# Performance work log

Measured on AMD Instinct MI355X. Metric: run time of the kernel, lower is better.

## Reference

```python
import jax, jax.numpy as jnp
import numpy as np


def setup_inputs() -> dict:
    key = jax.random.key(0)
    ks = jax.random.split(key, 6)
    B, S, F = 8, 2048, 1024
    scale = 1.0 / np.sqrt(F)
    return {
        "query": jax.random.normal(ks[0], (B, S, F), dtype=jnp.float32),
        "key": jax.random.normal(ks[1], (B, S, F), dtype=jnp.float32),
        "value": jax.random.normal(ks[2], (B, S, F), dtype=jnp.float32),
        "Wq": jax.random.normal(ks[3], (F, F), dtype=jnp.float32) * scale,
        "Wk": jax.random.normal(ks[4], (F, F), dtype=jnp.float32) * scale,
        "Wv": jax.random.normal(ks[5], (F, F), dtype=jnp.float32) * scale,
    }


def reference(query, key, value, Wq, Wk, Wv):
    # nn.Linear(bias=False): x @ W.T, W is [out, in]
    q_t = jnp.einsum('bsf,gf->bsg', query, Wq)
    k_t = jnp.einsum('bsf,gf->bsg', key, Wk)
    v_t = jnp.einsum('bsf,gf->bsg', value, Wv)
    F = k_t.shape[-1]
    scale = jnp.asarray(1.0, q_t.dtype) / jnp.sqrt(jnp.asarray(F, q_t.dtype))
    attn = jnp.einsum('bij,bkj->bik', q_t, k_t) * scale  # [B, S, S]
    # original uses nn.Softmax(dim=1): softmax over the query (i) axis
    attn = jax.nn.softmax(attn, axis=1)
    # 'bii,bij->bij': diagonal of attn scales rows of v_t
    diag = jnp.diagonal(attn, axis1=1, axis2=2)  # [B, S]
    proj = diag[:, :, None] * v_t  # [B, S, F]
    return proj
```

## Files before the change

### kernel.cpp

```cpp
#include <hip/hip_runtime.h>


typedef _Float16 f16x8 __attribute__((ext_vector_type(8)));
typedef float    f32x4 __attribute__((ext_vector_type(4)));

#define COLIC 8
#define SCALE 0.03125f

typedef __attribute__((address_space(1))) const unsigned int g_u32_t;
typedef __attribute__((address_space(3))) unsigned int l_u32_t;

__device__ __forceinline__ void gload16(const _Float16* g, _Float16* l) {
  __builtin_amdgcn_global_load_lds((g_u32_t*)g, (l_u32_t*)l, 16, 0, 0);
}

__device__ __forceinline__ void stage_tile64(const _Float16* gbase, int ldk,
                                             _Float16* lds, int w, int lane) {
#pragma unroll
  for (int c = 0; c < 4; ++c) {
    const int blk = c * 4 + w;
    const int o = (blk << 10) + (lane << 4);
    const int row = o >> 7;
    const int colb = (o & 127) ^ ((row & 7) << 4);
    gload16(gbase + (size_t)row * ldk + (colb >> 1), lds + (blk << 9));
  }
}

struct Conv3Args {
  const float* src[3];
  _Float16* dst[3];
};
__global__ __launch_bounds__(256)
void conv3_f32_f16(Conv3Args a, int n8) {
  const float* __restrict__ src = a.src[blockIdx.y];
  _Float16* __restrict__ dst = a.dst[blockIdx.y];
  for (int i = blockIdx.x * 256 + threadIdx.x; i < n8; i += gridDim.x * 256) {
    const float4 x = ((const float4*)src)[2 * i];
    const float4 y = ((const float4*)src)[2 * i + 1];
    f16x8 o;
    o[0] = (_Float16)x.x; o[1] = (_Float16)x.y;
    o[2] = (_Float16)x.z; o[3] = (_Float16)x.w;
    o[4] = (_Float16)y.x; o[5] = (_Float16)y.y;
    o[6] = (_Float16)y.z; o[7] = (_Float16)y.w;
    ((f16x8*)dst)[i] = o;
  }
}

struct Conv2Args {
  const float* src[2];
  _Float16* dst[2];
};
__global__ __launch_bounds__(256)
void convT_f32_f16(Conv2Args a) {
  __shared__ float Ts[64][65];
  const float* __restrict__ src = a.src[blockIdx.z];
  _Float16* __restrict__ dst = a.dst[blockIdx.z];
  const int g0 = blockIdx.x * 64, f0 = blockIdx.y * 64;
  const int tid = threadIdx.x;
  {
    const int r = tid >> 4;
    const int c4 = (tid & 15) << 2;
#pragma unroll
    for (int p = 0; p < 4; ++p) {
      const int row = p * 16 + r;
      const float4 v = *(const float4*)&src[(size_t)(g0 + row) * 1024 + f0 + c4];
      Ts[row][c4 + 0] = v.x; Ts[row][c4 + 1] = v.y;
      Ts[row][c4 + 2] = v.z; Ts[row][c4 + 3] = v.w;
    }
  }
  __syncthreads();
  {
    const int f = tid >> 3;
    const int gs = (tid & 7) << 3;
#pragma unroll
    for (int p = 0; p < 2; ++p) {
      const int fr = p * 32 + f;
      f16x8 v;
#pragma unroll
      for (int j = 0; j < 8; ++j) v[j] = (_Float16)Ts[gs + j][fr];
      *(f16x8*)&dst[(size_t)(f0 + fr) * 1024 + g0 + gs] = v;
    }
  }
}

template <int F16OUT>
__global__ __launch_bounds__(256)
void gemm_mfma(const _Float16* __restrict__ A, const _Float16* __restrict__ B,
               _Float16* __restrict__ C16, float* __restrict__ C32,
               const float* __restrict__ mpart, const float* __restrict__ lpart,
               const float* __restrict__ sdiag, int BSz,
               int M, int N, int Kd) {
  __shared__ __align__(16) _Float16 As[128 * 64];
  __shared__ __align__(16) _Float16 Bs[128 * 64];
  __shared__ float diagS[128];
  const int tid = threadIdx.x;
  const int w = tid >> 6, lane = tid & 63;
  const int wr = w >> 1, wc = w & 1;
  const int lr = lane & 15, kq = lane >> 4;
  const int swz = (lr & 7) << 4;
  const int bm = blockIdx.x * 128, bn = blockIdx.y * 128;

  if (!F16OUT && tid < 128) {
    const int row = bm + tid;
    float Mx = -3.0e38f;
#pragma unroll
    for (int c = 0; c < COLIC; ++c) Mx = fmaxf(Mx, mpart[(size_t)c * BSz + row]);
    float L = 0.0f;
#pragma unroll
    for (int c = 0; c < COLIC; ++c)
      L += lpart[(size_t)c * BSz + row] * __expf(mpart[(size_t)c * BSz + row] - Mx);
    diagS[tid] = __expf(sdiag[row] - Mx) / L;
  }

  f32x4 acc[4][4] = {};
  for (int k0 = 0; k0 < Kd; k0 += 64) {
    stage_tile64(A + (size_t)bm * Kd + k0, Kd, As, w, lane);
    stage_tile64(B + (size_t)bn * Kd + k0, Kd, Bs, w, lane);
    __syncthreads();
    f16x8 af[4][2], bf[4][2];
#pragma unroll
    for (int mi = 0; mi < 4; ++mi) {
      const int ro = (wr * 64 + mi * 16 + lr) << 7;
      af[mi][0] = *(const f16x8*)&As[(ro + ((kq * 16) ^ swz)) >> 1];
      af[mi][1] = *(const f16x8*)&As[(ro + ((64 + kq * 16) ^ swz)) >> 1];
    }
#pragma unroll
    for (int ni = 0; ni < 4; ++ni) {
      const int ro = (wc * 64 + ni * 16 + lr) << 7;
      bf[ni][0] = *(const f16x8*)&Bs[(ro + ((kq * 16) ^ swz)) >> 1];
      bf[ni][1] = *(const f16x8*)&Bs[(ro + ((64 + kq * 16) ^ swz)) >> 1];
    }
#pragma unroll
    for (int ks = 0; ks < 2; ++ks)
#pragma unroll
      for (int mi = 0; mi < 4; ++mi)
#pragma unroll
        for (int ni = 0; ni < 4; ++ni)
          acc[mi][ni] = __builtin_amdgcn_mfma_f32_16x16x32_f16(af[mi][ks], bf[ni][ks], acc[mi][ni], 0, 0, 0);
    __syncthreads();
  }
#pragma unroll
  for (int mi = 0; mi < 4; ++mi) {
#pragma unroll
    for (int j = 0; j < 4; ++j) {
      const int rloc = wr * 64 + mi * 16 + kq * 4 + j;
      const int row = bm + rloc;
      float s = 1.0f;
      if (!F16OUT) s = diagS[rloc];
#pragma unroll
      for (int ni = 0; ni < 4; ++ni) {
        const int col = bn + wc * 64 + ni * 16 + lr;
        if (F16OUT) C16[(size_t)row * N + col] = (_Float16)acc[mi][ni][j];
        else        C32[(size_t)row * N + col] = acc[mi][ni][j] * s;
      }
    }
  }
}

__global__ __launch_bounds__(256)
void col_stats_mfma(const _Float16* __restrict__ qt, const _Float16* __restrict__ kt,
                    float* __restrict__ mpart, float* __restrict__ lpart,
                    float* __restrict__ sdiag, int S, int Fd, int chunk) {
  __shared__ __align__(16) _Float16 Qs[128 * 64];
  __shared__ __align__(16) _Float16 Ks[128 * 64];
  __shared__ float redM[8][128];
  __shared__ float redL[8][128];
  const int t = blockIdx.x + 16 * (blockIdx.y + 8 * blockIdx.z);
  const int jb = ((t & 7) << 1) | ((t >> 3) & 1);
  const int rr = t >> 4;
  const int ic = rr & 7;
  const int b  = rr >> 3;
  const int j0 = jb * 128;
  const _Float16* Q = qt + (size_t)b * S * Fd;
  const _Float16* K = kt + (size_t)b * S * Fd;
  const int tid = threadIdx.x;
  const int w = tid >> 6, lane = tid & 63;
  const int wr = w >> 1, wc = w & 1;
  const int lr = lane & 15, kq = lane >> 4;
  const int swz = (lr & 7) << 4;

  float m[4], l[4];
#pragma unroll
  for (int ni = 0; ni < 4; ++ni) { m[ni] = -3.0e38f; l[ni] = 0.0f; }

  for (int it = 0; it < chunk >> 7; ++it) {
    const int i0 = ic * chunk + (it << 7);
    f32x4 acc[4][4] = {};
    for (int k0 = 0; k0 < Fd; k0 += 64) {
      stage_tile64(Q + (size_t)i0 * Fd + k0, Fd, Qs, w, lane);
      stage_tile64(K + (size_t)j0 * Fd + k0, Fd, Ks, w, lane);
      __syncthreads();
      f16x8 af[4][2], bf[4][2];
#pragma unroll
      for (int mi = 0; mi < 4; ++mi) {
        const int ro = (wr * 64 + mi * 16 + lr) << 7;
        af[mi][0] = *(const f16x8*)&Qs[(ro + ((kq * 16) ^ swz)) >> 1];
        af[mi][1] = *(const f16x8*)&Qs[(ro + ((64 + kq * 16) ^ swz)) >> 1];
      }
#pragma unroll
      for (int ni = 0; ni < 4; ++ni) {
        const int ro = (wc * 64 + ni * 16 + lr) << 7;
        bf[ni][0] = *(const f16x8*)&Ks[(ro + ((kq * 16) ^ swz)) >> 1];
        bf[ni][1] = *(const f16x8*)&Ks[(ro + ((64 + kq * 16) ^ swz)) >> 1];
      }
#pragma unroll
      for (int ks = 0; ks < 2; ++ks)
#pragma unroll
        for (int mi = 0; mi < 4; ++mi)
#pragma unroll
          for (int ni = 0; ni < 4; ++ni)
            acc[mi][ni] = __builtin_amdgcn_mfma_f32_16x16x32_f16(af[mi][ks], bf[ni][ks], acc[mi][ni], 0, 0, 0);
      __syncthreads();
    }
    if (i0 == j0 && wr == wc && (lr >> 2) == kq) {
      const int j = lr & 3;
#pragma unroll
      for (int jj = 0; jj < 4; ++jj)
        sdiag[(size_t)b * S + j0 + wc * 64 + jj * 16 + lr] = acc[jj][jj][j] * SCALE;
    }
#pragma unroll
    for (int ni = 0; ni < 4; ++ni) {
      float tm = -3.0e38f;
#pragma unroll
      for (int mi = 0; mi < 4; ++mi)
#pragma unroll
        for (int jj = 0; jj < 4; ++jj) tm = fmaxf(tm, acc[mi][ni][jj]);
      tm *= SCALE;
      const float mn = fmaxf(m[ni], tm);
      float add = 0.0f;
#pragma unroll
      for (int mi = 0; mi < 4; ++mi)
#pragma unroll
        for (int jj = 0; jj < 4; ++jj) add += __expf(acc[mi][ni][jj] * SCALE - mn);
      l[ni] = l[ni] * __expf(m[ni] - mn) + add;
      m[ni] = mn;
    }
  }
  __syncthreads();
  const int p = wr * 4 + kq;
#pragma unroll
  for (int ni = 0; ni < 4; ++ni) {
    const int col = wc * 64 + ni * 16 + lr;
    redM[p][col] = m[ni];
    redL[p][col] = l[ni];
  }
  __syncthreads();
  if (tid < 128) {
    float M = -3.0e38f;
#pragma unroll
    for (int q = 0; q < 8; ++q) M = fmaxf(M, redM[q][tid]);
    float L = 0.0f;
#pragma unroll
    for (int q = 0; q < 8; ++q) L += redL[q][tid] * __expf(redM[q][tid] - M);
    const size_t idx = ((size_t)ic * 8 + b) * S + j0 + tid;
    mpart[idx] = M;
    lpart[idx] = L;
  }
}

extern "C" void kernel_launch(void* const* d_in, const int* in_sizes, int n_in,
                              void* d_out, int out_size, void* d_ws, size_t ws_size,
                              hipStream_t stream) {
  const float* query = (const float*)d_in[0];
  const float* key   = (const float*)d_in[1];
  const float* value = (const float*)d_in[2];
  const float* Wq    = (const float*)d_in[3];
  const float* Wk    = (const float*)d_in[4];
  const float* Wv    = (const float*)d_in[5];

  const int F = 1024;
  const int BS = in_sizes[0] / F;
  const int B = 8;
  const int S = BS / B;

  _Float16* q16   = (_Float16*)d_ws;
  _Float16* k16   = q16 + (size_t)BS * F;
  _Float16* v16   = k16 + (size_t)BS * F;
  _Float16* wqT16 = v16 + (size_t)BS * F;
  _Float16* wkT16 = wqT16 + (size_t)F * F;
  _Float16* wv16  = wkT16 + (size_t)F * F;
  _Float16* W2h   = wv16 + (size_t)F * F;
  float* mpart = (float*)(W2h + (size_t)F * F);
  float* lpart = mpart + (size_t)COLIC * BS;
  float* sdiag = lpart + (size_t)COLIC * BS;

  _Float16* kt2 = (_Float16*)d_out;

  const dim3 blk(256);
  const int n8x = BS * F / 8, n8w = F * F / 8;

  Conv3Args ax; ax.src[0] = query; ax.src[1] = key; ax.src[2] = value;
  ax.dst[0] = q16; ax.dst[1] = k16; ax.dst[2] = v16;
  conv3_f32_f16<<<dim3(2048, 3), blk, 0, stream>>>(ax, n8x);

  Conv3Args av; av.src[0] = Wv; av.dst[0] = wv16;
  conv3_f32_f16<<<dim3(512, 1), blk, 0, stream>>>(av, n8w);

  Conv2Args at; at.src[0] = Wq; at.src[1] = Wk;
  at.dst[0] = wqT16; at.dst[1] = wkT16;
  convT_f32_f16<<<dim3(16, 16, 2), blk, 0, stream>>>(at);

  gemm_mfma<1><<<dim3(8, 8), blk, 0, stream>>>(wqT16, wkT16, W2h, (float*)nullptr,
                                               (const float*)nullptr, (const float*)nullptr,
                                               (const float*)nullptr, 0, F, F, F);

  gemm_mfma<1><<<dim3(BS / 128, F / 128), blk, 0, stream>>>(k16, W2h, kt2, (float*)nullptr,
                                               (const float*)nullptr, (const float*)nullptr,
                                               (const float*)nullptr, 0, BS, F, F);

  const dim3 sgrid(S / 128, COLIC, B);
  col_stats_mfma<<<sgrid, blk, 0, stream>>>(q16, kt2, mpart, lpart, sdiag,
                                            S, F, S / COLIC);

  gemm_mfma<0><<<dim3(BS / 128, F / 128), blk, 0, stream>>>(v16, wv16, (_Float16*)nullptr,
                                               (float*)d_out, mpart, lpart, sdiag,
                                               BS, BS, F, F);
}
```

Before: 270.8 us.

## Widen col_stats tiles to 256 key columns with 512-thread blocks

The column-statistics kernel now covers 256 key columns per block using 8 waves (2x4) instead of 128 columns with 4 waves, so each staged Q tile is reused across twice as many key columns. Staging, the diagonal extraction and the per-column reduction are adapted to the wider tile, and the custom block-index swizzle is dropped in favour of a plain grid mapping. This halves redundant Q loads but raises LDS use and block size, which can lower occupancy and changes L2 locality.

New measurement: 275.7 us. Within noise of the previous version (+1.8%).

```diff
diff --git a/kernel.cpp b/kernel.cpp
--- a/kernel.cpp
+++ b/kernel.cpp
@@ -19,6 +19,19 @@
 #pragma unroll
   for (int c = 0; c < 4; ++c) {
     const int blk = c * 4 + w;
+    const int o = (blk << 10) + (lane << 4);
+    const int row = o >> 7;
+    const int colb = (o & 127) ^ ((row & 7) << 4);
+    gload16(gbase + (size_t)row * ldk + (colb >> 1), lds + (blk << 9));
+  }
+}
+
+template <int CH>
+__device__ __forceinline__ void stage_rows8(const _Float16* gbase, int ldk,
+                                            _Float16* lds, int w8, int lane) {
+#pragma unroll
+  for (int c = 0; c < CH; ++c) {
+    const int blk = c * 8 + w8;
     const int o = (blk << 10) + (lane << 4);
     const int row = o >> 7;
     const int colb = (o & 127) ^ ((row & 7) << 4);
@@ -157,25 +170,21 @@
   }
 }
 
-__global__ __launch_bounds__(256)
+__global__ __launch_bounds__(512)
 void col_stats_mfma(const _Float16* __restrict__ qt, const _Float16* __restrict__ kt,
                     float* __restrict__ mpart, float* __restrict__ lpart,
                     float* __restrict__ sdiag, int S, int Fd, int chunk) {
   __shared__ __align__(16) _Float16 Qs[128 * 64];
-  __shared__ __align__(16) _Float16 Ks[128 * 64];
-  __shared__ float redM[8][128];
-  __shared__ float redL[8][128];
-  const int t = blockIdx.x + 16 * (blockIdx.y + 8 * blockIdx.z);
-  const int jb = ((t & 7) << 1) | ((t >> 3) & 1);
-  const int rr = t >> 4;
-  const int ic = rr & 7;
-  const int b  = rr >> 3;
-  const int j0 = jb * 128;
+  __shared__ __align__(16) _Float16 Ks[256 * 64];
+  __shared__ float redM[8][256];
+  __shared__ float redL[8][256];
+  const int b = blockIdx.z, jb = blockIdx.x, ic = blockIdx.y;
+  const int j0b = jb * 256;
   const _Float16* Q = qt + (size_t)b * S * Fd;
   const _Float16* K = kt + (size_t)b * S * Fd;
   const int tid = threadIdx.x;
   const int w = tid >> 6, lane = tid & 63;
-  const int wr = w >> 1, wc = w & 1;
+  const int wr = w >> 2, wc = w & 3;
   const int lr = lane & 15, kq = lane >> 4;
   const int swz = (lr & 7) << 4;
 
@@ -187,8 +196,8 @@
     const int i0 = ic * chunk + (it << 7);
     f32x4 acc[4][4] = {};
     for (int k0 = 0; k0 < Fd; k0 += 64) {
-      stage_tile64(Q + (size_t)i0 * Fd + k0, Fd, Qs, w, lane);
-      stage_tile64(K + (size_t)j0 * Fd + k0, Fd, Ks, w, lane);
+      stage_rows8<2>(Q + (size_t)i0 * Fd + k0, Fd, Qs, w, lane);
+      stage_rows8<4>(K + (size_t)j0b * Fd + k0, Fd, Ks, w, lane);
       __syncthreads();
       f16x8 af[4][2], bf[4][2];
 #pragma unroll
@@ -212,11 +221,14 @@
             acc[mi][ni] = __builtin_amdgcn_mfma_f32_16x16x32_f16(af[mi][ks], bf[ni][ks], acc[mi][ni], 0, 0, 0);
       __syncthreads();
     }
-    if (i0 == j0 && wr == wc && (lr >> 2) == kq) {
-      const int j = lr & 3;
-#pragma unroll
-      for (int jj = 0; jj < 4; ++jj)
-        sdiag[(size_t)b * S + j0 + wc * 64 + jj * 16 + lr] = acc[jj][jj][j] * SCALE;
+    if (i0 >= j0b && i0 < j0b + 256) {
+      const int jh = (i0 - j0b) >> 7;
+      if ((wc >> 1) == jh && (wc & 1) == wr && (lr >> 2) == kq) {
+        const int j = lr & 3;
+#pragma unroll
+        for (int mi = 0; mi < 4; ++mi)
+          sdiag[(size_t)b * S + j0b + wc * 64 + mi * 16 + lr] = acc[mi][mi][j] * SCALE;
+      }
     }
 #pragma unroll
     for (int ni = 0; ni < 4; ++ni) {
@@ -245,14 +257,14 @@
     redL[p][col] = l[ni];
   }
   __syncthreads();
-  if (tid < 128) {
+  if (tid < 256) {
     float M = -3.0e38f;
 #pragma unroll
     for (int q = 0; q < 8; ++q) M = fmaxf(M, redM[q][tid]);
     float L = 0.0f;
 #pragma unroll
     for (int q = 0; q < 8; ++q) L += redL[q][tid] * __expf(redM[q][tid] - M);
-    const size_t idx = ((size_t)ic * 8 + b) * S + j0 + tid;
+    const size_t idx = ((size_t)ic * gridDim.z + b) * S + j0b + tid;
     mpart[idx] = M;
     lpart[idx] = L;
   }
@@ -308,9 +320,9 @@
                                                (const float*)nullptr, (const float*)nullptr,
                                                (const float*)nullptr, 0, BS, F, F);
 
-  const dim3 sgrid(S / 128, COLIC, B);
-  col_stats_mfma<<<sgrid, blk, 0, stream>>>(q16, kt2, mpart, lpart, sdiag,
-                                            S, F, S / COLIC);
+  const dim3 sgrid(S / 256, COLIC, B);
+  col_stats_mfma<<<sgrid, dim3(512), 0, stream>>>(q16, kt2, mpart, lpart, sdiag,
+                                                  S, F, S / COLIC);
 
   gemm_mfma<0><<<dim3(BS / 128, F / 128), blk, 0, stream>>>(v16, wv16, (_Float16*)nullptr,
                                                (float*)d_out, mpart, lpart, sdiag,
```

## Flatten col_stats loops and overlap softmax stats with next tile loads

Applied to the files above, without the earlier changes.

The nested row-tile and k-step loops become one flattened loop. The online max/sum update for the previous row tile now runs after the first k-slice of the next tile has been issued, so exp work can hide load latency. The block-index swizzle that grouped column blocks is replaced by direct blockIdx mapping, which may change L2 locality. The partial-index stride now uses gridDim.z, and the final __syncthreads before the reduction was removed. This relies on the loop's trailing barrier, and the hardcoded ks mask assumes Fd=1024.

After: 632.9 us. 134% more time.

```diff
diff --git a/kernel.cpp b/kernel.cpp
--- a/kernel.cpp
+++ b/kernel.cpp
@@ -165,11 +165,7 @@
   __shared__ __align__(16) _Float16 Ks[128 * 64];
   __shared__ float redM[8][128];
   __shared__ float redL[8][128];
-  const int t = blockIdx.x + 16 * (blockIdx.y + 8 * blockIdx.z);
-  const int jb = ((t & 7) << 1) | ((t >> 3) & 1);
-  const int rr = t >> 4;
-  const int ic = rr & 7;
-  const int b  = rr >> 3;
+  const int b = blockIdx.z, jb = blockIdx.x, ic = blockIdx.y;
   const int j0 = jb * 128;
   const _Float16* Q = qt + (size_t)b * S * Fd;
   const _Float16* K = kt + (size_t)b * S * Fd;
@@ -183,35 +179,13 @@
 #pragma unroll
   for (int ni = 0; ni < 4; ++ni) { m[ni] = -3.0e38f; l[ni] = 0.0f; }
 
-  for (int it = 0; it < chunk >> 7; ++it) {
-    const int i0 = ic * chunk + (it << 7);
-    f32x4 acc[4][4] = {};
-    for (int k0 = 0; k0 < Fd; k0 += 64) {
-      stage_tile64(Q + (size_t)i0 * Fd + k0, Fd, Qs, w, lane);
-      stage_tile64(K + (size_t)j0 * Fd + k0, Fd, Ks, w, lane);
-      __syncthreads();
-      f16x8 af[4][2], bf[4][2];
-#pragma unroll
-      for (int mi = 0; mi < 4; ++mi) {
-        const int ro = (wr * 64 + mi * 16 + lr) << 7;
-        af[mi][0] = *(const f16x8*)&Qs[(ro + ((kq * 16) ^ swz)) >> 1];
-        af[mi][1] = *(const f16x8*)&Qs[(ro + ((64 + kq * 16) ^ swz)) >> 1];
-      }
-#pragma unroll
-      for (int ni = 0; ni < 4; ++ni) {
-        const int ro = (wc * 64 + ni * 16 + lr) << 7;
-        bf[ni][0] = *(const f16x8*)&Ks[(ro + ((kq * 16) ^ swz)) >> 1];
-        bf[ni][1] = *(const f16x8*)&Ks[(ro + ((64 + kq * 16) ^ swz)) >> 1];
-      }
-#pragma unroll
-      for (int ks = 0; ks < 2; ++ks)
-#pragma unroll
-        for (int mi = 0; mi < 4; ++mi)
-#pragma unroll
-          for (int ni = 0; ni < 4; ++ni)
-            acc[mi][ni] = __builtin_amdgcn_mfma_f32_16x16x32_f16(af[mi][ks], bf[ni][ks], acc[mi][ni], 0, 0, 0);
-      __syncthreads();
-    }
+  const int nit = chunk >> 7;
+  const int ksteps = Fd >> 6;
+  const int G = nit * ksteps;
+
+  f32x4 acc[4][4];
+
+  auto finish = [&](int i0) {
     if (i0 == j0 && wr == wc && (lr >> 2) == kq) {
       const int j = lr & 3;
 #pragma unroll
@@ -235,8 +209,47 @@
       l[ni] = l[ni] * __expf(m[ni] - mn) + add;
       m[ni] = mn;
     }
-  }
-  __syncthreads();
+  };
+
+  for (int gg = 0; gg < G; ++gg) {
+    const int it = gg >> 4;
+    const int ks = gg & 15;
+    const int i0 = ic * chunk + (it << 7);
+    const int k0 = ks << 6;
+    stage_tile64(Q + (size_t)i0 * Fd + k0, Fd, Qs, w, lane);
+    stage_tile64(K + (size_t)j0 * Fd + k0, Fd, Ks, w, lane);
+    if (ks == 0) {
+      if (gg > 0) finish(ic * chunk + ((it - 1) << 7));
+#pragma unroll
+      for (int mi = 0; mi < 4; ++mi)
+#pragma unroll
+        for (int ni = 0; ni < 4; ++ni) acc[mi][ni] = (f32x4){0.f, 0.f, 0.f, 0.f};
+    }
+    __syncthreads();
+    f16x8 af[4][2], bf[4][2];
+#pragma unroll
+    for (int mi = 0; mi < 4; ++mi) {
+      const int ro = (wr * 64 + mi * 16 + lr) << 7;
+      af[mi][0] = *(const f16x8*)&Qs[(ro + ((kq * 16) ^ swz)) >> 1];
+      af[mi][1] = *(const f16x8*)&Qs[(ro + ((64 + kq * 16) ^ swz)) >> 1];
+    }
+#pragma unroll
+    for (int ni = 0; ni < 4; ++ni) {
+      const int ro = (wc * 64 + ni * 16 + lr) << 7;
+      bf[ni][0] = *(const f16x8*)&Ks[(ro + ((kq * 16) ^ swz)) >> 1];
+      bf[ni][1] = *(const f16x8*)&Ks[(ro + ((64 + kq * 16) ^ swz)) >> 1];
+    }
+#pragma unroll
+    for (int ks2 = 0; ks2 < 2; ++ks2)
+#pragma unroll
+      for (int mi = 0; mi < 4; ++mi)
+#pragma unroll
+        for (int ni = 0; ni < 4; ++ni)
+          acc[mi][ni] = __builtin_amdgcn_mfma_f32_16x16x32_f16(af[mi][ks2], bf[ni][ks2], acc[mi][ni], 0, 0, 0);
+    __syncthreads();
+  }
+  finish(ic * chunk + ((nit - 1) << 7));
+
   const int p = wr * 4 + kq;
 #pragma unroll
   for (int ni = 0; ni < 4; ++ni) {
@@ -252,7 +265,7 @@
     float L = 0.0f;
 #pragma unroll
     for (int q = 0; q < 8; ++q) L += redL[q][tid] * __expf(redM[q][tid] - M);
-    const size_t idx = ((size_t)ic * 8 + b) * S + j0 + tid;
+    const size_t idx = ((size_t)ic * gridDim.z + b) * S + j0 + tid;
     mpart[idx] = M;
     lpart[idx] = L;
   }
```
